# Kernel tuning notes

Measured on AMD Instinct MI355X. Metric: run time of the kernel, lower is better.

## Reference

```python
import jax, jax.numpy as jnp
import numpy as np

HIDDEN = 1024
NUM_HEADS = 16
HEAD_DIM = HIDDEN // NUM_HEADS  # 64


def setup_inputs() -> dict:
    key = jax.random.key(0)
    ks = jax.random.split(key, 9)
    B, S = 2, 512
    scale = 0.02
    return {
        "x": jax.random.normal(ks[0], (B, S, HIDDEN), dtype=jnp.float32),
        "Wq": jax.random.normal(ks[1], (HIDDEN, HIDDEN), dtype=jnp.float32) * scale,
        "bq": jnp.zeros((HIDDEN,), dtype=jnp.float32),
        "Wk": jax.random.normal(ks[2], (HIDDEN, HIDDEN), dtype=jnp.float32) * scale,
        "bk": jnp.zeros((HIDDEN,), dtype=jnp.float32),
        "Wv": jax.random.normal(ks[3], (HIDDEN, HIDDEN), dtype=jnp.float32) * scale,
        "bv": jnp.zeros((HIDDEN,), dtype=jnp.float32),
        "Wo": jax.random.normal(ks[4], (HIDDEN, HIDDEN), dtype=jnp.float32) * scale,
        "bo": jnp.zeros((HIDDEN,), dtype=jnp.float32),
    }


def reference(x, Wq, bq, Wk, bk, Wv, bv, Wo, bo):
    B, S, D = x.shape
    H, hd = NUM_HEADS, HEAD_DIM
    q = x @ Wq + bq  # [B,S,D]
    k = x @ Wk + bk
    v = x @ Wv + bv
    # split_heads(query): [B,S,H,hd] -> [B,H,S,hd]
    q = q.reshape(B, S, H, hd).transpose(0, 2, 1, 3)
    # split_heads(key/value, head_num=1): view(B,-1,1,hd) -> [B,S*H,1,hd] -> [B,1,S*H,hd]
    k = k.reshape(B, S * H, 1, hd).transpose(0, 2, 1, 3)
    v = v.reshape(B, S * H, 1, hd).transpose(0, 2, 1, 3)
    # scores: [B,H,S,hd] @ [B,1,hd,S*H] -> [B,H,S,S*H]
    scores = jnp.einsum('bhsd,bukd->bhsk', q, k) / jnp.sqrt(jnp.float32(hd))
    probs = jax.nn.softmax(scores, axis=-1)
    # out: [B,H,S,S*H] @ [B,1,S*H,hd] -> [B,H,S,hd]
    out = jnp.einsum('bhsk,bukd->bhsd', probs, v)
    # faithful to source: transpose(-1,-2) then view(B,-1,hidden)
    out = jnp.swapaxes(out, -1, -2).reshape(B, -1, D)  # [B,S,D] (scrambled layout, as in source)
    return out @ Wo + bo
```

## Files before the change

kernel.cpp:

```cpp
#include <hip/hip_runtime.h>

typedef float f4 __attribute__((ext_vector_type(4)));
typedef float f32x16 __attribute__((ext_vector_type(16)));
typedef __bf16 v8bf __attribute__((ext_vector_type(8)));
typedef unsigned short u16x8 __attribute__((ext_vector_type(8)));
typedef unsigned u32x4 __attribute__((ext_vector_type(4)));

#define MFMA32(a, b, c) __builtin_amdgcn_mfma_f32_32x32x16_bf16(a, b, c, 0, 0, 0)
#define QSCALE 0.18033688011112042f

#if __has_builtin(__builtin_amdgcn_exp2f)
#define EXP2(x) __builtin_amdgcn_exp2f(x)
#else
#define EXP2(x) exp2f(x)
#endif

#define GLDS(src, dst)                                                        \
  __builtin_amdgcn_global_load_lds(                                           \
      (const __attribute__((address_space(1))) unsigned int*)(src),           \
      (__attribute__((address_space(3))) unsigned int*)(dst), 16, 0, 0)

__device__ __forceinline__ unsigned short f2bf(float f) {
  unsigned u = __builtin_bit_cast(unsigned, f);
  u += 0x7FFFu + ((u >> 16) & 1u);
  return (unsigned short)(u >> 16);
}
__device__ __forceinline__ float bf2f(unsigned short h) {
  unsigned u = ((unsigned)h) << 16;
  return __builtin_bit_cast(float, u);
}
__device__ __forceinline__ unsigned cvt_pk_bf16(float lo, float hi) {
  unsigned r;
  asm("v_cvt_pk_bf16_f32 %0, %1, %2" : "=v"(r) : "v"(lo), "v"(hi));
  return r;
}
__device__ __forceinline__ void plane32_swap(unsigned& x, unsigned& y) {
  asm("v_permlane32_swap_b32 %0, %1" : "+v"(x), "+v"(y));
}

__global__ __launch_bounds__(256) void wconv(
    const float* __restrict__ Wq, const float* __restrict__ Wk,
    const float* __restrict__ Wv, const float* __restrict__ Wo,
    unsigned short* __restrict__ wt) {
  __shared__ __align__(16) float T[64][65];
  const int tid = threadIdx.x, z = blockIdx.z;
  const int k0 = blockIdx.y << 6, n0 = blockIdx.x << 6;
  const float* W = (z == 0) ? Wq : (z == 1) ? Wk : (z == 2) ? Wv : Wo;
  const float scale = (z == 0) ? QSCALE : 1.0f;
  {
    const int r = tid >> 2, c4 = (tid & 3) << 4;
    const float* src = W + (size_t)(k0 + r) * 1024 + n0 + c4;
#pragma unroll
    for (int u = 0; u < 4; ++u) {
      f4 t4 = *(const f4*)(src + (u << 2));
      T[c4 + (u << 2) + 0][r] = t4[0];
      T[c4 + (u << 2) + 1][r] = t4[1];
      T[c4 + (u << 2) + 2][r] = t4[2];
      T[c4 + (u << 2) + 3][r] = t4[3];
    }
  }
  __syncthreads();
  const int n = tid >> 2, kc = (tid & 3) << 4;
  unsigned short* dst = wt + ((size_t)z << 20) + (size_t)(n0 + n) * 1024 + k0 + kc;
  u16x8 o0, o1;
#pragma unroll
  for (int u = 0; u < 8; ++u) {
    o0[u] = f2bf(T[n][kc + u] * scale);
    o1[u] = f2bf(T[n][kc + 8 + u] * scale);
  }
  *(u16x8*)dst = o0;
  *(u16x8*)(dst + 8) = o1;
}

__global__ __launch_bounds__(256) void xconv(const float* __restrict__ x,
                                             unsigned short* __restrict__ xbf) {
  const int i = (blockIdx.x * 256 + threadIdx.x) << 3;
  f4 a = *(const f4*)(x + i);
  f4 b = *(const f4*)(x + i + 4);
  u16x8 o;
#pragma unroll
  for (int u = 0; u < 4; ++u) {
    o[u] = f2bf(a[u]);
    o[u + 4] = f2bf(b[u]);
  }
  *(u16x8*)(xbf + i) = o;
}

template <int MODE>
__device__ __forceinline__ void gemm_core(const unsigned short* __restrict__ A,
                                          const unsigned short* __restrict__ Bw,
                                          const float* __restrict__ bias,
                                          void* __restrict__ dst,
                                          float bscale = 1.0f) {
  __shared__ __align__(16) char lds[32768];
  const int tid = threadIdx.x, lane = tid & 63, w = tid >> 6;
  const int l31 = lane & 31, hi = lane >> 5;
  const int wm = w >> 1, wn = w & 1;
  const int m0 = blockIdx.y << 7, n0 = blockIdx.x << 7;

  f32x16 acc[2][2];
#pragma unroll
  for (int i = 0; i < 2; ++i)
#pragma unroll
    for (int j = 0; j < 2; ++j)
#pragma unroll
      for (int r = 0; r < 16; ++r) acc[i][j][r] = 0.f;

  auto stage = [&](int buf, int k0) {
    char* base = lds + buf * 16384;
#pragma unroll
    for (int j = 0; j < 4; ++j) {
      const int c = w * 4 + j;
      const int cm = c & 7;
      const unsigned short* gsrc = (c < 8) ? A : Bw;
      const int r0 = (c < 8) ? m0 : n0;
      const int row = cm * 8 + (lane >> 3);
      const int u = (lane & 7) ^ (row & 7);
      const unsigned short* src =
          gsrc + (size_t)(r0 + row + ((u >> 2) << 6)) * 1024 + k0 + ((u & 3) << 3);
      char* ldst = base + ((c < 8) ? 0 : 8192) + cm * 1024;
      GLDS(src, ldst);
    }
  };

  stage(0, 0);
  for (int ks = 0; ks < 32; ++ks) {
    const int buf = ks & 1;
    __syncthreads();
    if (ks < 31) stage(buf ^ 1, (ks + 1) * 32);
    const char* base = lds + buf * 16384;
#pragma unroll
    for (int kc = 0; kc < 2; ++kc) {
      v8bf a[2], b[2];
#pragma unroll
      for (int i = 0; i < 2; ++i) {
        const int r = i * 32 + l31;
        const int ua = wm * 4 + kc * 2 + hi;
        a[i] = *(const v8bf*)(base + r * 128 + ((ua ^ (r & 7)) << 4));
        const int ub = wn * 4 + kc * 2 + hi;
        b[i] = *(const v8bf*)(base + 8192 + r * 128 + ((ub ^ (r & 7)) << 4));
      }
#pragma unroll
      for (int im = 0; im < 2; ++im)
#pragma unroll
        for (int in = 0; in < 2; ++in)
          acc[im][in] = MFMA32(a[im], b[in], acc[im][in]);
    }
  }

  if (MODE == 0) {
    unsigned short* q = (unsigned short*)dst;
#pragma unroll
    for (int in = 0; in < 2; ++in) {
      const int n = n0 + wn * 64 + in * 32 + l31;
      const float bv = bias[n] * bscale;
      const int h = n >> 6, d = n & 63;
#pragma unroll
      for (int im = 0; im < 2; ++im)
#pragma unroll
        for (int r = 0; r < 16; ++r) {
          const int m = m0 + wm * 64 + im * 32 + (r & 3) + ((r >> 2) << 3) + (hi << 2);
          const int bb = m >> 9, s = m & 511;
          q[((size_t)((bb * 16 + h) * 512 + s) << 6) + d] = f2bf(acc[im][in][r] + bv);
        }
    }
  } else if (MODE == 1) {
    unsigned short* vt = (unsigned short*)dst;
#pragma unroll
    for (int im = 0; im < 2; ++im)
#pragma unroll
      for (int r = 0; r < 16; ++r) {
        const int m = m0 + wm * 64 + im * 32 + (r & 3) + ((r >> 2) << 3) + (hi << 2);
        const float bv = bias[m];
        const int h = m >> 6, dd = m & 63;
#pragma unroll
        for (int in = 0; in < 2; ++in) {
          const int n = n0 + wn * 64 + in * 32 + l31;
          const int bb = n >> 9, s = n & 511;
          vt[((size_t)((bb * 16 + h) * 64 + dd) << 9) + s] = f2bf(acc[im][in][r] + bv);
        }
      }
  } else {
    float* of = (float*)dst;
#pragma unroll
    for (int in = 0; in < 2; ++in) {
      const int n = n0 + wn * 64 + in * 32 + l31;
      const float bv = bias[n];
#pragma unroll
      for (int im = 0; im < 2; ++im)
#pragma unroll
        for (int r = 0; r < 16; ++r) {
          const int m = m0 + wm * 64 + im * 32 + (r & 3) + ((r >> 2) << 3) + (hi << 2);
          of[(size_t)m * 1024 + n] = acc[im][in][r] + bv;
        }
    }
  }
}

__global__ __launch_bounds__(256) void gemm_qk(
    const unsigned short* __restrict__ xbf, const unsigned short* __restrict__ wt,
    const float* __restrict__ bq, const float* __restrict__ bk,
    unsigned short* __restrict__ qbf, unsigned short* __restrict__ kbf) {
  if (blockIdx.z == 0)
    gemm_core<0>(xbf, wt, bq, qbf, QSCALE);
  else
    gemm_core<0>(xbf, wt + (1u << 20), bk, kbf, 1.0f);
}

__global__ __launch_bounds__(256) void gemm_vT(
    const unsigned short* __restrict__ wvT, const unsigned short* __restrict__ xbf,
    const float* __restrict__ bv, unsigned short* __restrict__ vtbf) {
  gemm_core<1>(wvT, xbf, bv, vtbf, 1.0f);
}

__global__ __launch_bounds__(256) void gemm_out(
    const unsigned short* __restrict__ scr, const unsigned short* __restrict__ woT,
    const float* __restrict__ bo, float* __restrict__ out) {
  gemm_core<2>(scr, woT, bo, out, 1.0f);
}

__global__ __launch_bounds__(256) void attn_mfma(
    const unsigned short* __restrict__ qbf, const unsigned short* __restrict__ kbf,
    const unsigned short* __restrict__ vtbf, unsigned short* __restrict__ Ep,
    float* __restrict__ Lp) {
  __shared__ __align__(16) char smem[35328];
  const int tid = threadIdx.x, lane = tid & 63, w = tid >> 6;
  const int l31 = lane & 31, hi = lane >> 5;
  const int b = blockIdx.z, h = blockIdx.y;
  const int qt = blockIdx.x >> 1, ks = blockIdx.x & 1;
  const int qh = w & 1, kh = w >> 1;
  const int key0 = ks * 4096 + kh * 2048;

  const unsigned short* kb = kbf + ((size_t)b << 19);
  const unsigned short* vb = vtbf + ((size_t)b << 19);

  v8bf Qf[4];
  {
    const unsigned short* qg =
        qbf + ((size_t)((b * 16 + h) * 512 + qt * 64 + qh * 32 + l31) << 6) + hi * 8;
#pragma unroll
    for (int kc = 0; kc < 4; ++kc)
      Qf[kc] = __builtin_bit_cast(v8bf, *(const u16x8*)(qg + kc * 16));
  }

  f32x16 acc0, acc1;
#pragma unroll
  for (int r = 0; r < 16; ++r) { acc0[r] = 0.f; acc1[r] = 0.f; }
  float lp = 0.f;

  auto stage = [&](int buf, int it) {
    const int c0 = key0 + it * 32;
#pragma unroll
    for (int j = 0; j < 4; ++j) {
      const int row = j * 8 + (lane >> 3);
      const int u = (lane & 7) ^ (row & 7);
      if (qh == 0) {
        const unsigned short* src = kb + ((size_t)(c0 + row) << 6) + (u << 3);
        GLDS(src, smem + (buf * 2 + kh) * 4096 + j * 1024);
      } else {
        const int hk = c0 >> 9, s0 = c0 & 511;
        const int d = row + ((u >> 2) << 5);
        const unsigned short* src =
            vb + ((size_t)(hk * 64 + d) << 9) + s0 + ((u & 3) << 3);
        GLDS(src, smem + 16384 + (buf * 2 + kh) * 4096 + j * 1024);
      }
    }
  };

  stage(0, 0);
  __syncthreads();

  for (int it = 0; it < 64; ++it) {
    const int cur = it & 1;
    if (it < 63) stage(cur ^ 1, it + 1);

    const char* Kt = smem + (cur * 2 + kh) * 4096;
    const char* Vt = smem + 16384 + (cur * 2 + kh) * 4096;

    f32x16 C;
#pragma unroll
    for (int r = 0; r < 16; ++r) C[r] = 0.f;
#pragma unroll
    for (int kc = 0; kc < 4; ++kc) {
      v8bf ak = *(const v8bf*)(Kt + l31 * 128 + (((kc * 2 + hi) ^ (l31 & 7)) << 4));
      C = MFMA32(ak, Qf[kc], C);
    }

    float p[16];
#pragma unroll
    for (int r = 0; r < 16; ++r) {
      p[r] = EXP2(C[r]);
      lp += p[r];
    }
    unsigned pk0 = cvt_pk_bf16(p[0], p[1]), pk1 = cvt_pk_bf16(p[2], p[3]);
    unsigned pk2 = cvt_pk_bf16(p[4], p[5]), pk3 = cvt_pk_bf16(p[6], p[7]);
    unsigned pk4 = cvt_pk_bf16(p[8], p[9]), pk5 = cvt_pk_bf16(p[10], p[11]);
    unsigned pk6 = cvt_pk_bf16(p[12], p[13]), pk7 = cvt_pk_bf16(p[14], p[15]);
    plane32_swap(pk0, pk2);
    plane32_swap(pk1, pk3);
    plane32_swap(pk4, pk6);
    plane32_swap(pk5, pk7);
    const v8bf pa0 = __builtin_bit_cast(v8bf, (u32x4){pk0, pk1, pk2, pk3});
    const v8bf pa1 = __builtin_bit_cast(v8bf, (u32x4){pk4, pk5, pk6, pk7});

#pragma unroll
    for (int half = 0; half < 2; ++half) {
      v8bf bv0 = *(const v8bf*)(Vt + l31 * 128 +
                                (((half * 4 + hi) ^ (l31 & 7)) << 4));
      v8bf bv1 = *(const v8bf*)(Vt + l31 * 128 +
                                (((half * 4 + 2 + hi) ^ (l31 & 7)) << 4));
      if (half == 0) {
        acc0 = MFMA32(pa0, bv0, acc0);
        acc0 = MFMA32(pa1, bv1, acc0);
      } else {
        acc1 = MFMA32(pa0, bv0, acc1);
        acc1 = MFMA32(pa1, bv1, acc1);
      }
    }
    __syncthreads();
  }

  lp += __shfl_xor(lp, 32);

  __syncthreads();
  float* Ef = (float*)smem;
  float* Lf = (float*)(smem + 34816);
#pragma unroll
  for (int r = 0; r < 16; ++r) {
    const int q = qh * 32 + (r & 3) + ((r >> 2) << 3) + (hi << 2);
    Ef[(kh * 64 + l31) * 68 + q] = acc0[r];
    Ef[(kh * 64 + l31 + 32) * 68 + q] = acc1[r];
  }
  if (hi == 0) Lf[kh * 64 + qh * 32 + l31] = lp;
  __syncthreads();

  const size_t pb = (size_t)(((b * 16 + h) * 8 + qt) * 2 + ks);
  {
    const int q = tid >> 2, dch = (tid & 3) << 4;
    u16x8 o0, o1;
#pragma unroll
    for (int u = 0; u < 8; ++u) {
      o0[u] = f2bf(Ef[(dch + u) * 68 + q] + Ef[(64 + dch + u) * 68 + q]);
      o1[u] = f2bf(Ef[(dch + 8 + u) * 68 + q] + Ef[(64 + dch + 8 + u) * 68 + q]);
    }
    unsigned short* ep = Ep + (pb << 12) + (q << 6) + dch;
    *(u16x8*)ep = o0;
    *(u16x8*)(ep + 8) = o1;
  }
  if (tid < 64) Lp[(pb << 6) + tid] = Lf[tid] + Lf[64 + tid];
}

__global__ __launch_bounds__(256) void merge_k(const unsigned short* __restrict__ Ep,
                                               const float* __restrict__ Lp,
                                               unsigned short* __restrict__ scr) {
  const int tid = threadIdx.x;
  const int qt = blockIdx.x, h = blockIdx.y, b = blockIdx.z;
  const size_t eb = (size_t)(((b * 16 + h) * 8 + qt) * 2);
  const int d = tid & 63, qc = (tid >> 6) << 4;
  u16x8 o0, o1;
#pragma unroll
  for (int j = 0; j < 16; ++j) {
    const int q = qc + j;
    const float e = bf2f(Ep[(eb << 12) + (q << 6) + d]) +
                    bf2f(Ep[((eb + 1) << 12) + (q << 6) + d]);
    const float l = Lp[(eb << 6) + q] + Lp[((eb + 1) << 6) + q];
    const unsigned short v = f2bf(e / l);
    if (j < 8) o0[j] = v; else o1[j - 8] = v;
  }
  unsigned short* dst = scr + ((size_t)((b * 16 + h) * 64 + d) << 9) + qt * 64 + qc;
  *(u16x8*)dst = o0;
  *(u16x8*)(dst + 8) = o1;
}

extern "C" void kernel_launch(void* const* d_in, const int* in_sizes, int n_in,
                              void* d_out, int out_size, void* d_ws, size_t ws_size,
                              hipStream_t stream) {
  const float* x  = (const float*)d_in[0];
  const float* Wq = (const float*)d_in[1];
  const float* bq = (const float*)d_in[2];
  const float* Wk = (const float*)d_in[3];
  const float* bk = (const float*)d_in[4];
  const float* Wv = (const float*)d_in[5];
  const float* bv = (const float*)d_in[6];
  const float* Wo = (const float*)d_in[7];
  const float* bo = (const float*)d_in[8];
  float* out = (float*)d_out;

  char* wsb = (char*)d_ws;
  unsigned short* xbf  = (unsigned short*)wsb;
  unsigned short* scr  = (unsigned short*)wsb;
  unsigned short* qbf  = (unsigned short*)(wsb + (2u << 20));
  unsigned short* kbf  = (unsigned short*)(wsb + (4u << 20));
  unsigned short* vtbf = (unsigned short*)(wsb + (6u << 20));
  unsigned short* wt   = (unsigned short*)(wsb + (8u << 20));
  unsigned short* Ep   = (unsigned short*)(wsb + (8u << 20));
  float*          Lp   = (float*)(wsb + (12u << 20));
  unsigned short* wvT  = wt + (2u << 20);
  unsigned short* woT  = wt + (3u << 20);

  wconv<<<dim3(16, 16, 4), 256, 0, stream>>>(Wq, Wk, Wv, Wo, wt);
  xconv<<<dim3(512), 256, 0, stream>>>(x, xbf);
  gemm_qk<<<dim3(8, 8, 2), 256, 0, stream>>>(xbf, wt, bq, bk, qbf, kbf);
  gemm_vT<<<dim3(8, 8), 256, 0, stream>>>(wvT, xbf, bv, vtbf);
  attn_mfma<<<dim3(16, 16, 2), 256, 0, stream>>>(qbf, kbf, vtbf, Ep, Lp);
  merge_k<<<dim3(8, 16, 2), 256, 0, stream>>>(Ep, Lp, scr);
  gemm_out<<<dim3(8, 8), 256, 0, stream>>>(scr, woT, bo, out);
}
```

Before: 195.5 us.

## Merge prep kernels, fuse QKV GEMMs, shrink GEMM tiles, triple-buffer attention

The weight and input bf16 conversions now run as one launch, and the Q/K/V projections run in a single kernel instead of two. GEMM tiles shrink from 128x128 to 128x64, doubling the block count so more compute units stay busy. The attention kernel gets a three-stage buffered pipeline with explicit vmcnt waits in place of full syncthreads, plus an XCD-aware block-index remap meant to improve L2 locality. Together these aim to cut launch overhead, raise occupancy and overlap memory loads with compute, at the cost of more LDS per attention block and less data reuse per GEMM tile.

```diff
diff --git a/kernel.cpp b/kernel.cpp
--- a/kernel.cpp
+++ b/kernel.cpp
@@ -38,52 +38,52 @@
   asm("v_permlane32_swap_b32 %0, %1" : "+v"(x), "+v"(y));
 }
 
-__global__ __launch_bounds__(256) void wconv(
+__global__ __launch_bounds__(256) void prep(
     const float* __restrict__ Wq, const float* __restrict__ Wk,
     const float* __restrict__ Wv, const float* __restrict__ Wo,
-    unsigned short* __restrict__ wt) {
-  __shared__ __align__(16) float T[64][65];
-  const int tid = threadIdx.x, z = blockIdx.z;
-  const int k0 = blockIdx.y << 6, n0 = blockIdx.x << 6;
-  const float* W = (z == 0) ? Wq : (z == 1) ? Wk : (z == 2) ? Wv : Wo;
-  const float scale = (z == 0) ? QSCALE : 1.0f;
-  {
-    const int r = tid >> 2, c4 = (tid & 3) << 4;
-    const float* src = W + (size_t)(k0 + r) * 1024 + n0 + c4;
+    const float* __restrict__ x, unsigned short* __restrict__ wt,
+    unsigned short* __restrict__ xbf) {
+  const int id = blockIdx.x, tid = threadIdx.x;
+  if (id < 1024) {
+    __shared__ __align__(16) float T[64][65];
+    const int n0 = (id & 15) << 6, k0 = ((id >> 4) & 15) << 6, z = id >> 8;
+    const float* W = (z == 0) ? Wq : (z == 1) ? Wk : (z == 2) ? Wv : Wo;
+    const float scale = (z == 0) ? QSCALE : 1.0f;
+    {
+      const int r = tid >> 2, c4 = (tid & 3) << 4;
+      const float* src = W + (size_t)(k0 + r) * 1024 + n0 + c4;
+#pragma unroll
+      for (int u = 0; u < 4; ++u) {
+        f4 t4 = *(const f4*)(src + (u << 2));
+        T[c4 + (u << 2) + 0][r] = t4[0];
+        T[c4 + (u << 2) + 1][r] = t4[1];
+        T[c4 + (u << 2) + 2][r] = t4[2];
+        T[c4 + (u << 2) + 3][r] = t4[3];
+      }
+    }
+    __syncthreads();
+    const int n = tid >> 2, kc = (tid & 3) << 4;
+    unsigned short* dst = wt + ((size_t)z << 20) + (size_t)(n0 + n) * 1024 + k0 + kc;
+    u16x8 o0, o1;
+#pragma unroll
+    for (int u = 0; u < 8; ++u) {
+      o0[u] = f2bf(T[n][kc + u] * scale);
+      o1[u] = f2bf(T[n][kc + 8 + u] * scale);
+    }
+    *(u16x8*)dst = o0;
+    *(u16x8*)(dst + 8) = o1;
+  } else {
+    const int i = ((id - 1024) * 256 + tid) << 3;
+    f4 a = *(const f4*)(x + i);
+    f4 b = *(const f4*)(x + i + 4);
+    u16x8 o;
 #pragma unroll
     for (int u = 0; u < 4; ++u) {
-      f4 t4 = *(const f4*)(src + (u << 2));
-      T[c4 + (u << 2) + 0][r] = t4[0];
-      T[c4 + (u << 2) + 1][r] = t4[1];
-      T[c4 + (u << 2) + 2][r] = t4[2];
-      T[c4 + (u << 2) + 3][r] = t4[3];
-    }
-  }
-  __syncthreads();
-  const int n = tid >> 2, kc = (tid & 3) << 4;
-  unsigned short* dst = wt + ((size_t)z << 20) + (size_t)(n0 + n) * 1024 + k0 + kc;
-  u16x8 o0, o1;
-#pragma unroll
-  for (int u = 0; u < 8; ++u) {
-    o0[u] = f2bf(T[n][kc + u] * scale);
-    o1[u] = f2bf(T[n][kc + 8 + u] * scale);
-  }
-  *(u16x8*)dst = o0;
-  *(u16x8*)(dst + 8) = o1;
-}
-
-__global__ __launch_bounds__(256) void xconv(const float* __restrict__ x,
-                                             unsigned short* __restrict__ xbf) {
-  const int i = (blockIdx.x * 256 + threadIdx.x) << 3;
-  f4 a = *(const f4*)(x + i);
-  f4 b = *(const f4*)(x + i + 4);
-  u16x8 o;
-#pragma unroll
-  for (int u = 0; u < 4; ++u) {
-    o[u] = f2bf(a[u]);
-    o[u + 4] = f2bf(b[u]);
-  }
-  *(u16x8*)(xbf + i) = o;
+      o[u] = f2bf(a[u]);
+      o[u + 4] = f2bf(b[u]);
+    }
+    *(u16x8*)(xbf + i) = o;
+  }
 }
 
 template <int MODE>
@@ -92,34 +92,38 @@
                                           const float* __restrict__ bias,
                                           void* __restrict__ dst,
                                           float bscale = 1.0f) {
-  __shared__ __align__(16) char lds[32768];
+  __shared__ __align__(16) char lds[24576];
   const int tid = threadIdx.x, lane = tid & 63, w = tid >> 6;
   const int l31 = lane & 31, hi = lane >> 5;
   const int wm = w >> 1, wn = w & 1;
-  const int m0 = blockIdx.y << 7, n0 = blockIdx.x << 7;
-
-  f32x16 acc[2][2];
+  const int m0 = blockIdx.y << 7, n0 = blockIdx.x << 6;
+
+  f32x16 acc[2];
 #pragma unroll
   for (int i = 0; i < 2; ++i)
 #pragma unroll
-    for (int j = 0; j < 2; ++j)
-#pragma unroll
-      for (int r = 0; r < 16; ++r) acc[i][j][r] = 0.f;
+    for (int r = 0; r < 16; ++r) acc[i][r] = 0.f;
 
   auto stage = [&](int buf, int k0) {
-    char* base = lds + buf * 16384;
-#pragma unroll
-    for (int j = 0; j < 4; ++j) {
-      const int c = w * 4 + j;
-      const int cm = c & 7;
-      const unsigned short* gsrc = (c < 8) ? A : Bw;
-      const int r0 = (c < 8) ? m0 : n0;
-      const int row = cm * 8 + (lane >> 3);
-      const int u = (lane & 7) ^ (row & 7);
-      const unsigned short* src =
-          gsrc + (size_t)(r0 + row + ((u >> 2) << 6)) * 1024 + k0 + ((u & 3) << 3);
-      char* ldst = base + ((c < 8) ? 0 : 8192) + cm * 1024;
-      GLDS(src, ldst);
+    char* base = lds + buf * 12288;
+#pragma unroll
+    for (int j = 0; j < 3; ++j) {
+      const int c = w * 3 + j;
+      const int t = lane & 7;
+      if (c < 8) {
+        const int row = c * 8 + (lane >> 3);
+        const int u = t ^ (row & 7);
+        const unsigned short* src =
+            A + (size_t)(m0 + row + ((u >> 2) << 6)) * 1024 + k0 + ((u & 3) << 3);
+        GLDS(src, base + c * 1024);
+      } else {
+        const int cm = c - 8;
+        const int row = cm * 8 + (lane >> 3);
+        const int u = t ^ (row & 7);
+        const unsigned short* src =
+            Bw + (size_t)(n0 + row + ((u >> 2) << 5)) * 1024 + k0 + ((u & 3) << 3);
+        GLDS(src, base + 8192 + cm * 1024);
+      }
     }
   };
 
@@ -128,44 +132,37 @@
     const int buf = ks & 1;
     __syncthreads();
     if (ks < 31) stage(buf ^ 1, (ks + 1) * 32);
-    const char* base = lds + buf * 16384;
+    const char* base = lds + buf * 12288;
 #pragma unroll
     for (int kc = 0; kc < 2; ++kc) {
-      v8bf a[2], b[2];
-#pragma unroll
-      for (int i = 0; i < 2; ++i) {
-        const int r = i * 32 + l31;
+      const int ub = wn * 4 + kc * 2 + hi;
+      v8bf b = *(const v8bf*)(base + 8192 + l31 * 128 + ((ub ^ (l31 & 7)) << 4));
+#pragma unroll
+      for (int im = 0; im < 2; ++im) {
+        const int r = im * 32 + l31;
         const int ua = wm * 4 + kc * 2 + hi;
-        a[i] = *(const v8bf*)(base + r * 128 + ((ua ^ (r & 7)) << 4));
-        const int ub = wn * 4 + kc * 2 + hi;
-        b[i] = *(const v8bf*)(base + 8192 + r * 128 + ((ub ^ (r & 7)) << 4));
-      }
-#pragma unroll
-      for (int im = 0; im < 2; ++im)
-#pragma unroll
-        for (int in = 0; in < 2; ++in)
-          acc[im][in] = MFMA32(a[im], b[in], acc[im][in]);
-    }
-  }
-
+        v8bf a = *(const v8bf*)(base + r * 128 + ((ua ^ (r & 7)) << 4));
+        acc[im] = MFMA32(a, b, acc[im]);
+      }
+    }
+  }
+
+  const int n = n0 + wn * 32 + l31;
   if (MODE == 0) {
     unsigned short* q = (unsigned short*)dst;
-#pragma unroll
-    for (int in = 0; in < 2; ++in) {
-      const int n = n0 + wn * 64 + in * 32 + l31;
-      const float bv = bias[n] * bscale;
-      const int h = n >> 6, d = n & 63;
-#pragma unroll
-      for (int im = 0; im < 2; ++im)
-#pragma unroll
-        for (int r = 0; r < 16; ++r) {
-          const int m = m0 + wm * 64 + im * 32 + (r & 3) + ((r >> 2) << 3) + (hi << 2);
-          const int bb = m >> 9, s = m & 511;
-          q[((size_t)((bb * 16 + h) * 512 + s) << 6) + d] = f2bf(acc[im][in][r] + bv);
-        }
-    }
+    const float bv = bias[n] * bscale;
+    const int h = n >> 6, d = n & 63;
+#pragma unroll
+    for (int im = 0; im < 2; ++im)
+#pragma unroll
+      for (int r = 0; r < 16; ++r) {
+        const int m = m0 + wm * 64 + im * 32 + (r & 3) + ((r >> 2) << 3) + (hi << 2);
+        const int bb = m >> 9, s = m & 511;
+        q[((size_t)((bb * 16 + h) * 512 + s) << 6) + d] = f2bf(acc[im][r] + bv);
+      }
   } else if (MODE == 1) {
     unsigned short* vt = (unsigned short*)dst;
+    const int bb = n >> 9, s = n & 511;
 #pragma unroll
     for (int im = 0; im < 2; ++im)
 #pragma unroll
@@ -173,44 +170,33 @@
         const int m = m0 + wm * 64 + im * 32 + (r & 3) + ((r >> 2) << 3) + (hi << 2);
         const float bv = bias[m];
         const int h = m >> 6, dd = m & 63;
-#pragma unroll
-        for (int in = 0; in < 2; ++in) {
-          const int n = n0 + wn * 64 + in * 32 + l31;
-          const int bb = n >> 9, s = n & 511;
-          vt[((size_t)((bb * 16 + h) * 64 + dd) << 9) + s] = f2bf(acc[im][in][r] + bv);
-        }
+        vt[((size_t)((bb * 16 + h) * 64 + dd) << 9) + s] = f2bf(acc[im][r] + bv);
       }
   } else {
     float* of = (float*)dst;
-#pragma unroll
-    for (int in = 0; in < 2; ++in) {
-      const int n = n0 + wn * 64 + in * 32 + l31;
-      const float bv = bias[n];
-#pragma unroll
-      for (int im = 0; im < 2; ++im)
-#pragma unroll
-        for (int r = 0; r < 16; ++r) {
-          const int m = m0 + wm * 64 + im * 32 + (r & 3) + ((r >> 2) << 3) + (hi << 2);
-          of[(size_t)m * 1024 + n] = acc[im][in][r] + bv;
-        }
-    }
-  }
-}
-
-__global__ __launch_bounds__(256) void gemm_qk(
+    const float bv = bias[n];
+#pragma unroll
+    for (int im = 0; im < 2; ++im)
+#pragma unroll
+      for (int r = 0; r < 16; ++r) {
+        const int m = m0 + wm * 64 + im * 32 + (r & 3) + ((r >> 2) << 3) + (hi << 2);
+        of[(size_t)m * 1024 + n] = acc[im][r] + bv;
+      }
+  }
+}
+
+__global__ __launch_bounds__(256) void gemm_qkv(
     const unsigned short* __restrict__ xbf, const unsigned short* __restrict__ wt,
     const float* __restrict__ bq, const float* __restrict__ bk,
-    unsigned short* __restrict__ qbf, unsigned short* __restrict__ kbf) {
+    const float* __restrict__ bv,
+    unsigned short* __restrict__ qbf, unsigned short* __restrict__ kbf,
+    unsigned short* __restrict__ vtbf) {
   if (blockIdx.z == 0)
     gemm_core<0>(xbf, wt, bq, qbf, QSCALE);
+  else if (blockIdx.z == 1)
+    gemm_core<0>(xbf, wt + (1u << 20), bk, kbf, 1.0f);
   else
-    gemm_core<0>(xbf, wt + (1u << 20), bk, kbf, 1.0f);
-}
-
-__global__ __launch_bounds__(256) void gemm_vT(
-    const unsigned short* __restrict__ wvT, const unsigned short* __restrict__ xbf,
-    const float* __restrict__ bv, unsigned short* __restrict__ vtbf) {
-  gemm_core<1>(wvT, xbf, bv, vtbf, 1.0f);
+    gemm_core<1>(wt + (2u << 20), xbf, bv, vtbf, 1.0f);
 }
 
 __global__ __launch_bounds__(256) void gemm_out(
@@ -223,11 +209,14 @@
     const unsigned short* __restrict__ qbf, const unsigned short* __restrict__ kbf,
     const unsigned short* __restrict__ vtbf, unsigned short* __restrict__ Ep,
     float* __restrict__ Lp) {
-  __shared__ __align__(16) char smem[35328];
+  __shared__ __align__(16) char smem[49152];
   const int tid = threadIdx.x, lane = tid & 63, w = tid >> 6;
   const int l31 = lane & 31, hi = lane >> 5;
-  const int b = blockIdx.z, h = blockIdx.y;
-  const int qt = blockIdx.x >> 1, ks = blockIdx.x & 1;
+  const int f = blockIdx.x;
+  const int xcd = f & 7, g = f >> 3;
+  const int b = xcd >> 2;
+  const int u0 = ((xcd & 3) << 6) + g;
+  const int h = u0 & 15, qt = (u0 >> 4) & 7, ks = u0 >> 7;
   const int qh = w & 1, kh = w >> 1;
   const int key0 = ks * 4096 + kh * 2048;
 
@@ -242,6 +231,8 @@
     for (int kc = 0; kc < 4; ++kc)
       Qf[kc] = __builtin_bit_cast(v8bf, *(const u16x8*)(qg + kc * 16));
   }
+  __builtin_amdgcn_sched_barrier(0);
+  asm volatile("s_waitcnt vmcnt(0)" ::: "memory");
 
   f32x16 acc0, acc1;
 #pragma unroll
@@ -262,20 +253,23 @@
         const int d = row + ((u >> 2) << 5);
         const unsigned short* src =
             vb + ((size_t)(hk * 64 + d) << 9) + s0 + ((u & 3) << 3);
-        GLDS(src, smem + 16384 + (buf * 2 + kh) * 4096 + j * 1024);
+        GLDS(src, smem + 24576 + (buf * 2 + kh) * 4096 + j * 1024);
       }
     }
   };
 
   stage(0, 0);
-  __syncthreads();
-
+  stage(1, 1);
+  asm volatile("s_waitcnt vmcnt(4)" ::: "memory");
+  __builtin_amdgcn_s_barrier();
+  __builtin_amdgcn_sched_barrier(0);
+
+  int cur = 0, nx1 = 1, nx2 = 2;
   for (int it = 0; it < 64; ++it) {
-    const int cur = it & 1;
-    if (it < 63) stage(cur ^ 1, it + 1);
+    if (it < 62) stage(nx2, it + 2);
 
     const char* Kt = smem + (cur * 2 + kh) * 4096;
-    const char* Vt = smem + 16384 + (cur * 2 + kh) * 4096;
+    const char* Vt = smem + 24576 + (cur * 2 + kh) * 4096;
 
     f32x16 C;
 #pragma unroll
@@ -305,10 +299,8 @@
 
 #pragma unroll
     for (int half = 0; half < 2; ++half) {
-      v8bf bv0 = *(const v8bf*)(Vt + l31 * 128 +
-                                (((half * 4 + hi) ^ (l31 & 7)) << 4));
-      v8bf bv1 = *(const v8bf*)(Vt + l31 * 128 +
-                                (((half * 4 + 2 + hi) ^ (l31 & 7)) << 4));
+      v8bf bv0 = *(const v8bf*)(Vt + l31 * 128 + (((half * 4 + hi) ^ (l31 & 7)) << 4));
+      v8bf bv1 = *(const v8bf*)(Vt + l31 * 128 + (((half * 4 + 2 + hi) ^ (l31 & 7)) << 4));
       if (half == 0) {
         acc0 = MFMA32(pa0, bv0, acc0);
         acc0 = MFMA32(pa1, bv1, acc0);
@@ -317,7 +309,16 @@
         acc1 = MFMA32(pa1, bv1, acc1);
       }
     }
-    __syncthreads();
+
+    if (it < 63) {
+      if (it < 62)
+        asm volatile("s_waitcnt vmcnt(4)" ::: "memory");
+      else
+        asm volatile("s_waitcnt vmcnt(0)" ::: "memory");
+      __builtin_amdgcn_s_barrier();
+      __builtin_amdgcn_sched_barrier(0);
+    }
+    const int t = cur; cur = nx1; nx1 = nx2; nx2 = t;
   }
 
   lp += __shfl_xor(lp, 32);
@@ -395,14 +396,11 @@
   unsigned short* wt   = (unsigned short*)(wsb + (8u << 20));
   unsigned short* Ep   = (unsigned short*)(wsb + (8u << 20));
   float*          Lp   = (float*)(wsb + (12u << 20));
-  unsigned short* wvT  = wt + (2u << 20);
   unsigned short* woT  = wt + (3u << 20);
 
-  wconv<<<dim3(16, 16, 4), 256, 0, stream>>>(Wq, Wk, Wv, Wo, wt);
-  xconv<<<dim3(512), 256, 0, stream>>>(x, xbf);
-  gemm_qk<<<dim3(8, 8, 2), 256, 0, stream>>>(xbf, wt, bq, bk, qbf, kbf);
-  gemm_vT<<<dim3(8, 8), 256, 0, stream>>>(wvT, xbf, bv, vtbf);
-  attn_mfma<<<dim3(16, 16, 2), 256, 0, stream>>>(qbf, kbf, vtbf, Ep, Lp);
+  prep<<<dim3(1536), 256, 0, stream>>>(Wq, Wk, Wv, Wo, x, wt, xbf);
+  gemm_qkv<<<dim3(16, 8, 3), 256, 0, stream>>>(xbf, wt, bq, bk, bv, qbf, kbf, vtbf);
+  attn_mfma<<<dim3(512), 256, 0, stream>>>(qbf, kbf, vtbf, Ep, Lp);
   merge_k<<<dim3(8, 16, 2), 256, 0, stream>>>(Ep, Lp, scr);
-  gemm_out<<<dim3(8, 8), 256, 0, stream>>>(scr, woT, bo, out);
-}
+  gemm_out<<<dim3(16, 8), 256, 0, stream>>>(scr, woT, bo, out);
+}
```

Measured after the change: 180.0 us. -8.0%, faster.
